# Kernel tuning notes

Measured on AMD Instinct MI355X. Metric: run time of the kernel, lower is better.

## Reference

```python
import jax, jax.numpy as jnp
import numpy as np

D_H, HEAD, LAYER_IDX = 1024, 16, 11
D_ATTN = D_H // HEAD
BZ, LEN = 2, 2048


def setup_inputs() -> dict:
    key = jax.random.key(0)
    ks = jax.random.split(key, 8)
    s = 1.0 / np.sqrt(D_H)
    v = jax.random.normal(ks[0], (BZ, LEN, D_H), jnp.float32)
    k = jax.random.normal(ks[1], (BZ, LEN, D_H), jnp.float32)
    q = jax.random.normal(ks[2], (BZ, LEN, D_H), jnp.float32)
    # causal mask: 1.0 where attention is blocked (j > i)
    causal = jnp.triu(jnp.ones((LEN, LEN), jnp.float32), k=1)
    mask = jnp.broadcast_to(causal[None, None], (BZ, 1, LEN, LEN))
    Wv = jax.random.normal(ks[3], (D_H, D_H), jnp.float32) * s
    Wk = jax.random.normal(ks[4], (D_H, D_H), jnp.float32) * s
    Wq = jax.random.normal(ks[5], (D_H, D_H), jnp.float32) * s
    Wo = jax.random.normal(ks[6], (D_H, D_H), jnp.float32) * s
    bo = jnp.zeros((D_H,), jnp.float32)
    return {"v": v, "k": k, "q": q, "mask": mask,
            "Wv": Wv, "Wk": Wk, "Wq": Wq, "Wo": Wo, "bo": bo}


def _split_head(x):
    # (bz, len, d_h) -> (bz, head, len, d_attn)
    bz, L, _ = x.shape
    return x.reshape(bz, L, HEAD, D_ATTN).transpose(0, 2, 1, 3)


def reference(v, k, q, mask, Wv, Wk, Wq, Wo, bo):
    bz, len_q, _ = q.shape
    vh = _split_head(v @ Wv)  # (bz, head, len_k, d_attn)
    kh = _split_head(k @ Wk)
    qh = _split_head(q @ Wq)
    scale = 1.0 / jnp.sqrt(jnp.asarray(D_ATTN, jnp.float32))
    weight = jnp.einsum("bhqd,bhkd->bhqk", qh, kh) * scale
    weight = weight + mask * (-1e9)
    weight = weight / jnp.asarray(LAYER_IDX + 1, jnp.float32)
    attn = jax.nn.softmax(weight, axis=-1)  # dropout omitted (inference)
    out = jnp.einsum("bhqk,bhkd->bhqd", attn, vh)
    out = out.transpose(0, 2, 1, 3).reshape(bz, len_q, D_H)
    return out @ Wo + bo
```

## Files before the change

### kernel.cpp

```cpp
#include <hip/hip_runtime.h>
#include <hip/hip_fp16.h>

typedef _Float16 f16;
typedef _Float16 f16x4 __attribute__((ext_vector_type(4)));
typedef _Float16 f16x8 __attribute__((ext_vector_type(8)));
typedef float f32x4 __attribute__((ext_vector_type(4)));

#define D_H   1024
#define LEN   2048
#define BZ    2
#define NHEAD 16
#define DA    64
#define MTOK  (BZ * LEN)
#define KDIM  1024
#define ATT_SCALE (0.125f / 12.0f)

__device__ __forceinline__ void load_lds16(const f16* g, f16* l) {
  __builtin_amdgcn_global_load_lds((const __attribute__((address_space(1))) void*)g,
                                   (__attribute__((address_space(3))) void*)l,
                                   16, 0, 0);
}

#define FENCE() __asm__ volatile("" ::: "memory")

__global__ __launch_bounds__(256)
void k_prep(const float* __restrict__ W0, const float* __restrict__ W1,
            const float* __restrict__ W2, const float* __restrict__ W3,
            const float* __restrict__ xq, const float* __restrict__ xk,
            const float* __restrict__ xv,
            f16* __restrict__ T0, f16* __restrict__ T1,
            f16* __restrict__ T2, f16* __restrict__ T3,
            f16* __restrict__ q16, f16* __restrict__ k16,
            f16* __restrict__ v16) {
  const int z = blockIdx.z;
  const int tx = threadIdx.x, ty = threadIdx.y;
  if (z < 4) {
    const float* W = (z == 0) ? W0 : (z == 1) ? W1 : (z == 2) ? W2 : W3;
    f16* Wt = (z == 0) ? T0 : (z == 1) ? T1 : (z == 2) ? T2 : T3;
    __shared__ float tile[32][33];
    int bx = blockIdx.x, by = blockIdx.y;
#pragma unroll
    for (int s = 0; s < 4; ++s)
      tile[ty + 8 * s][tx] = W[(size_t)(by * 32 + ty + 8 * s) * D_H + bx * 32 + tx];
    __syncthreads();
#pragma unroll
    for (int s = 0; s < 4; ++s)
      Wt[(size_t)(bx * 32 + ty + 8 * s) * D_H + by * 32 + tx] =
          (f16)tile[tx][ty + 8 * s];
  } else {
    const float* in = (z == 4) ? xq : (z == 5) ? xk : xv;
    f16* out = (z == 4) ? q16 : (z == 5) ? k16 : v16;
    int tid = ty * 32 + tx;
    size_t base = ((size_t)(blockIdx.y * 32 + blockIdx.x)) * 4096 + tid * 16;
#pragma unroll
    for (int s = 0; s < 4; ++s) {
      float4 x = *(const float4*)(in + base + s * 4);
      f16x4 o; o[0] = (f16)x.x; o[1] = (f16)x.y; o[2] = (f16)x.z; o[3] = (f16)x.w;
      *(f16x4*)(out + base + s * 4) = o;
    }
  }
}

#define BM2 256
#define BN2 256
#define BKT 64
#define NKT (KDIM / BKT)

__global__ __launch_bounds__(512, 2)
void k_gemm3(const f16* __restrict__ A0, const f16* __restrict__ A1,
             const f16* __restrict__ A2, const f16* __restrict__ W0,
             const f16* __restrict__ W1, const f16* __restrict__ W2,
             f16* __restrict__ O0, f16* __restrict__ O1, f16* __restrict__ O2) {
  __shared__ __align__(16) f16 smem3[65536];
  f16* As = smem3;
  f16* Bs = smem3 + 32768;
  const int z = blockIdx.z;
  const f16* A = (z == 0) ? A0 : (z == 1) ? A1 : A2;
  const f16* Bt = (z == 0) ? W0 : (z == 1) ? W1 : W2;
  f16* Out = (z == 0) ? O0 : (z == 1) ? O1 : O2;
  const int m0 = blockIdx.x * BM2, n0 = blockIdx.y * BN2;
  const int tid = threadIdx.x;
  const int wave = tid >> 6, lane = tid & 63;
  const int lc = lane & 15, quad = lane >> 4;
  const int wr = wave >> 2, wc = wave & 3;
  const f16* Ab = A + (size_t)m0 * KDIM;
  const f16* Bb = Bt + (size_t)n0 * KDIM;

  f32x4 acc[8][4] = {};

#define STAGE_HALF(g, ldsbase, kt, h)                                         \
  {                                                                           \
    _Pragma("unroll")                                                         \
    for (int r = 0; r < 2; ++r) {                                             \
      int idx = tid + r * 512;                                                \
      int row = (h) * 128 + (idx >> 3);                                       \
      int gch = (idx & 7) ^ (row & 7);                                        \
      load_lds16((g) + (size_t)row * KDIM + (kt) * BKT + gch * 8,             \
                 (ldsbase) + (h) * 8192 + idx * 8);                           \
    }                                                                         \
  }

#define READ_A(mh, kc)                                                        \
  _Pragma("unroll")                                                           \
  for (int i = 0; i < 4; ++i) {                                               \
    int row = wr * 128 + ((mh) * 4 + i) * 16 + lc;                            \
    int pc = ((kc) * 4 + quad) ^ (row & 7);                                   \
    af[i] = *(const f16x8*)&Ad[row * 64 + pc * 8];                            \
  }
#define READ_B(kc)                                                            \
  _Pragma("unroll")                                                           \
  for (int n = 0; n < 4; ++n) {                                               \
    int row = wc * 64 + n * 16 + lc;                                          \
    int pc = ((kc) * 4 + quad) ^ (row & 7);                                   \
    bf[n] = *(const f16x8*)&Bd[row * 64 + pc * 8];                            \
  }
#define MFMA_Q(mh)                                                            \
  FENCE(); __builtin_amdgcn_s_barrier();                                      \
  __asm__ volatile("s_waitcnt lgkmcnt(0)" ::: "memory");                      \
  __builtin_amdgcn_sched_barrier(0);                                          \
  __builtin_amdgcn_s_setprio(1);                                              \
  _Pragma("unroll")                                                           \
  for (int i = 0; i < 4; ++i)                                                 \
    _Pragma("unroll")                                                         \
    for (int n = 0; n < 4; ++n)                                               \
      acc[(mh) * 4 + i][n] = __builtin_amdgcn_mfma_f32_16x16x32_f16(          \
          af[i], bf[n], acc[(mh) * 4 + i][n], 0, 0, 0);                       \
  __builtin_amdgcn_s_setprio(0);                                              \
  FENCE(); __builtin_amdgcn_s_barrier(); FENCE();

  STAGE_HALF(Ab, As, 0, 0);
  STAGE_HALF(Ab, As, 0, 1);
  STAGE_HALF(Bb, Bs, 0, 0);
  STAGE_HALF(Bb, Bs, 0, 1);
  STAGE_HALF(Ab, As + 16384, 1, 0);
  __asm__ volatile("s_waitcnt vmcnt(2)" ::: "memory");
  __builtin_amdgcn_s_barrier();
  FENCE();

  for (int t = 0; t < NKT; ++t) {
    const f16* Ad = As + (t & 1) * 16384;
    const f16* Bd = Bs + (t & 1) * 16384;
    f16* AdW = As + (t & 1) * 16384;
    f16* Adn = As + ((t + 1) & 1) * 16384;
    f16* Bdn = Bs + ((t + 1) & 1) * 16384;
    const bool pf = (t + 1 < NKT);
    f16x8 af[4], bf[4];

    READ_A(0, 0); READ_B(0);
    if (pf) STAGE_HALF(Ab, Adn, t + 1, 1);
    MFMA_Q(0);

    READ_A(1, 0);
    if (pf) STAGE_HALF(Bb, Bdn, t + 1, 0);
    MFMA_Q(1);

    READ_A(0, 1); READ_B(1);
    if (pf) STAGE_HALF(Bb, Bdn, t + 1, 1);
    MFMA_Q(0);

    READ_A(1, 1);
    FENCE(); __builtin_amdgcn_s_barrier();
    __asm__ volatile("s_waitcnt lgkmcnt(0)" ::: "memory");
    __builtin_amdgcn_sched_barrier(0);
    __builtin_amdgcn_s_setprio(1);
#pragma unroll
    for (int i = 0; i < 4; ++i)
#pragma unroll
      for (int n = 0; n < 4; ++n)
        acc[4 + i][n] = __builtin_amdgcn_mfma_f32_16x16x32_f16(
            af[i], bf[n], acc[4 + i][n], 0, 0, 0);
    __builtin_amdgcn_s_setprio(0);
    if (t + 2 < NKT) {
      STAGE_HALF(Ab, AdW, t + 2, 0);
      __asm__ volatile("s_waitcnt vmcnt(2)" ::: "memory");
    } else if (pf) {
      __asm__ volatile("s_waitcnt vmcnt(0)" ::: "memory");
    }
    FENCE(); __builtin_amdgcn_s_barrier(); FENCE();
  }

  if (z <= 1) {
    f16* slice = smem3 + wave * 8192;
#pragma unroll
    for (int mi = 0; mi < 8; ++mi)
#pragma unroll
      for (int ni = 0; ni < 4; ++ni)
#pragma unroll
        for (int rr = 0; rr < 4; ++rr) {
          int tl = mi * 16 + quad * 4 + rr;
          int d = ni * 16 + lc;
          slice[tl * 64 + (((d >> 3) ^ (tl & 7)) << 3) + (d & 7)] =
              (f16)acc[mi][ni][rr];
        }
    __asm__ volatile("s_waitcnt lgkmcnt(0)" ::: "memory");
    const int h = (n0 >> 6) + wc;
    const int tokbase = m0 + wr * 128;
    const int b = tokbase >> 11, ib = tokbase & 2047;
#pragma unroll
    for (int s = 0; s < 16; ++s) {
      int u = lane + s * 64;
      int tl = u >> 3, ch = u & 7;
      f16x8 vv = *(const f16x8*)&slice[tl * 64 + ((ch ^ (tl & 7)) << 3)];
      *(f16x8*)(Out + ((size_t)((b << 4) + h) * LEN + ib + tl) * DA + ch * 8) = vv;
    }
  } else {
    f16* Ct = smem3;
#pragma unroll
    for (int e = 0; e < 2; ++e) {
      __syncthreads();
      if (wr == e) {
#pragma unroll
        for (int mi = 0; mi < 8; ++mi)
#pragma unroll
          for (int ni = 0; ni < 4; ++ni)
#pragma unroll
            for (int rr = 0; rr < 4; ++rr) {
              int tl = mi * 16 + quad * 4 + rr;
              int dl = wc * 64 + ni * 16 + lc;
              Ct[dl * 136 + tl] = (f16)acc[mi][ni][rr];
            }
      }
      __syncthreads();
      const int tokbase = m0 + e * 128;
      const int b = tokbase >> 11, j0 = tokbase & 2047;
#pragma unroll
      for (int s = 0; s < 8; ++s) {
        int u = tid + s * 512;
        int dl = u >> 4, ch = u & 15;
        f16x8 vv = *(const f16x8*)&Ct[dl * 136 + ch * 8];
        *(f16x8*)(Out + ((size_t)(b * 1024 + n0 + dl)) * LEN + j0 + ch * 8) = vv;
      }
    }
  }
}

#define OM 64
#define ON 128
#define BK 64
#define ONIT (KDIM / BK)
__global__ __launch_bounds__(256)
void k_gemm_out(const f16* __restrict__ A, const f16* __restrict__ Bt,
                float* __restrict__ Out, const float* __restrict__ bias) {
  __shared__ __align__(16) char smem[2 * (OM + ON) * BK * 2];
  f16* As = (f16*)smem;
  f16* Bs = As + 2 * OM * BK;
  const int m0 = blockIdx.x * OM, n0 = blockIdx.y * ON;
  const int tid = threadIdx.x;
  const int wave = tid >> 6, lane = tid & 63;
  const int lc = lane & 15, quad = lane >> 4;
  const int wm = (wave >> 1) * 32, wn = (wave & 1) * 64;
  const int swz = lc & 7;
  const f16* Abase = A + (size_t)m0 * KDIM;
  const f16* Bbase = Bt + (size_t)n0 * KDIM;

  f32x4 acc[2][4] = {};

#define STAGE_OUT(t)                                                          \
  {                                                                           \
    int k0s = (t) * BK;                                                       \
    f16* Ad = As + ((t) & 1) * (OM * BK);                                     \
    f16* Bd = Bs + ((t) & 1) * (ON * BK);                                     \
    _Pragma("unroll")                                                         \
    for (int r = 0; r < 2; ++r) {                                             \
      int idx = tid + r * 256;                                                \
      int row = idx >> 3, ch = idx & 7;                                       \
      int gch = ch ^ (row & 7);                                               \
      load_lds16(Abase + (size_t)row * KDIM + k0s + gch * 8, &Ad[idx * 8]);   \
    }                                                                         \
    _Pragma("unroll")                                                         \
    for (int r = 0; r < 4; ++r) {                                             \
      int idx = tid + r * 256;                                                \
      int row = idx >> 3, ch = idx & 7;                                       \
      int gch = ch ^ (row & 7);                                               \
      load_lds16(Bbase + (size_t)row * KDIM + k0s + gch * 8, &Bd[idx * 8]);   \
    }                                                                         \
  }

  STAGE_OUT(0);
  for (int t = 0; t < ONIT; ++t) {
    __syncthreads();
    if (t + 1 < ONIT) STAGE_OUT(t + 1);
    const f16* Ad = As + (t & 1) * (OM * BK);
    const f16* Bd = Bs + (t & 1) * (ON * BK);
#pragma unroll
    for (int kc = 0; kc < 2; ++kc) {
      f16x8 af[2], bf[4];
#pragma unroll
      for (int mi = 0; mi < 2; ++mi)
        af[mi] = *(const f16x8*)&Ad[(wm + mi * 16 + lc) * 64 +
                                    (((kc * 4 + quad) ^ swz) * 8)];
#pragma unroll
      for (int ni = 0; ni < 4; ++ni)
        bf[ni] = *(const f16x8*)&Bd[(wn + ni * 16 + lc) * 64 +
                                    (((kc * 4 + quad) ^ swz) * 8)];
#pragma unroll
      for (int mi = 0; mi < 2; ++mi)
#pragma unroll
        for (int ni = 0; ni < 4; ++ni)
          acc[mi][ni] = __builtin_amdgcn_mfma_f32_16x16x32_f16(
              af[mi], bf[ni], acc[mi][ni], 0, 0, 0);
    }
  }

  float* Ct = (float*)smem;
#pragma unroll
  for (int hf = 0; hf < 2; ++hf) {
    __syncthreads();
    if ((wave & 1) == hf) {
#pragma unroll
      for (int mi = 0; mi < 2; ++mi)
#pragma unroll
        for (int ni = 0; ni < 4; ++ni)
#pragma unroll
          for (int r = 0; r < 4; ++r) {
            int tok = wm + mi * 16 + quad * 4 + r;
            int d = ni * 16 + lc;
            Ct[tok * 68 + d] = acc[mi][ni][r];
          }
    }
    __syncthreads();
#pragma unroll
    for (int it = 0; it < 4; ++it) {
      int u = tid + it * 256;
      int tok = u >> 4, ch = u & 15;
      int gm = m0 + tok;
      int gc = n0 + hf * 64 + ch * 4;
      float4 bv = *(const float4*)(bias + gc);
      float4 cv = *(const float4*)&Ct[tok * 68 + ch * 4];
      float4 ov;
      ov.x = cv.x + bv.x; ov.y = cv.y + bv.y;
      ov.z = cv.z + bv.z; ov.w = cv.w + bv.w;
      *(float4*)(Out + (size_t)gm * D_H + gc) = ov;
    }
  }
}

__global__ __launch_bounds__(256, 4)
void k_attn(const f16* __restrict__ Qh, const f16* __restrict__ Kh,
            const f16* __restrict__ Vt, f16* __restrict__ O16) {
  __shared__ f16 Ks[2][64 * 64];
  __shared__ f16 Vs[2][64 * 64];
  __shared__ f16 Pw[4][16 * 64];
  const int tid = threadIdx.x;
  const int wave = tid >> 6, lane = tid & 63;
  const int lc = lane & 15, quad = lane >> 4;
  const int swz = lc & 7;
  const int bh = blockIdx.x & 31;
  const int qb = 31 - (blockIdx.x >> 5);
  const int i0 = qb * 64 + wave * 16;
  const int b = bh >> 4, h = bh & 15;
  const f16* Qb = Qh + (size_t)bh * LEN * DA;
  const f16* Kb = Kh + (size_t)bh * LEN * DA;
  const f16* Vb = Vt + (size_t)bh * DA * LEN;

  f16x8 aQ[2];
  const f16 qs = (f16)ATT_SCALE;
#pragma unroll
  for (int c = 0; c < 2; ++c) {
    aQ[c] = *(const f16x8*)(Qb + (size_t)(i0 + lc) * DA + c * 32 + quad * 8);
#pragma unroll
    for (int j = 0; j < 8; ++j) aQ[c][j] = aQ[c][j] * qs;
  }

  float lsum = 0.f;
  f32x4 accO[4] = {};
  f16* P = &Pw[wave][0];

  const int niter = qb + 1;

#pragma unroll
  for (int r = 0; r < 2; ++r) {
    int idx = tid + r * 256;
    int row = idx >> 3, ch = idx & 7;
    int gch = ch ^ (row & 7);
    load_lds16(Kb + (size_t)row * DA + gch * 8, &Ks[0][idx * 8]);
  }
#pragma unroll
  for (int r = 0; r < 2; ++r) {
    int idx = tid + r * 256;
    int row = idx >> 3, ch = idx & 7;
    int gch = ch ^ (row & 7);
    load_lds16(Vb + (size_t)row * LEN + gch * 8, &Vs[0][idx * 8]);
  }

  for (int t = 0; t < niter; ++t) {
    __syncthreads();
    if (t + 1 < niter) {
      int j0n = (t + 1) * 64, nb = (t + 1) & 1;
#pragma unroll
      for (int r = 0; r < 2; ++r) {
        int idx = tid + r * 256;
        int row = idx >> 3, ch = idx & 7;
        int gch = ch ^ (row & 7);
        load_lds16(Kb + (size_t)(j0n + row) * DA + gch * 8, &Ks[nb][idx * 8]);
      }
#pragma unroll
      for (int r = 0; r < 2; ++r) {
        int idx = tid + r * 256;
        int row = idx >> 3, ch = idx & 7;
        int gch = ch ^ (row & 7);
        load_lds16(Vb + (size_t)row * LEN + j0n + gch * 8, &Vs[nb][idx * 8]);
      }
    }
    const f16* ks = Ks[t & 1];
    const f16* vs = Vs[t & 1];

    f32x4 st[4] = {};
#pragma unroll
    for (int g = 0; g < 4; ++g)
#pragma unroll
      for (int c = 0; c < 2; ++c) {
        f16x8 aK = *(const f16x8*)&ks[(g * 16 + lc) * 64 +
                                      (((c * 4 + quad) ^ swz) * 8)];
        st[g] = __builtin_amdgcn_mfma_f32_16x16x32_f16(aK, aQ[c], st[g], 0, 0, 0);
      }
    float ev[4][4];
    if (t == niter - 1) {
      const int j0 = t * 64, q = i0 + lc;
#pragma unroll
      for (int g = 0; g < 4; ++g)
#pragma unroll
        for (int r = 0; r < 4; ++r) {
          int key = j0 + g * 16 + quad * 4 + r;
          float e = __expf(st[g][r]);
          e = (key > q) ? 0.f : e;
          lsum += e;
          ev[g][r] = e;
        }
    } else {
#pragma unroll
      for (int g = 0; g < 4; ++g)
#pragma unroll
        for (int r = 0; r < 4; ++r) {
          float e = __expf(st[g][r]);
          lsum += e;
          ev[g][r] = e;
        }
    }
#pragma unroll
    for (int g = 0; g < 4; ++g) {
      int c8 = ((g << 1) + (quad >> 1)) ^ swz;
      f16x4 pk;
      pk[0] = (f16)ev[g][0]; pk[1] = (f16)ev[g][1];
      pk[2] = (f16)ev[g][2]; pk[3] = (f16)ev[g][3];
      *(f16x4*)&P[lc * 64 + c8 * 8 + (quad & 1) * 4] = pk;
    }
    __asm__ volatile("s_waitcnt lgkmcnt(0)" ::: "memory");
    f16x8 aP[2];
#pragma unroll
    for (int c = 0; c < 2; ++c) {
      int c8 = (quad + 4 * c) ^ swz;
      aP[c] = *(const f16x8*)&P[lc * 64 + c8 * 8];
    }
#pragma unroll
    for (int dc = 0; dc < 4; ++dc) {
      f16x8 bV0 = *(const f16x8*)&vs[(dc * 16 + lc) * 64 + ((quad ^ swz) * 8)];
      f16x8 bV1 = *(const f16x8*)&vs[(dc * 16 + lc) * 64 + (((4 + quad) ^ swz) * 8)];
      accO[dc] = __builtin_amdgcn_mfma_f32_16x16x32_f16(aP[0], bV0, accO[dc], 0, 0, 0);
      accO[dc] = __builtin_amdgcn_mfma_f32_16x16x32_f16(aP[1], bV1, accO[dc], 0, 0, 0);
    }
  }

  lsum += __shfl_xor(lsum, 16, 64);
  lsum += __shfl_xor(lsum, 32, 64);
  float ls[4];
#pragma unroll
  for (int r = 0; r < 4; ++r) ls[r] = __shfl(lsum, quad * 4 + r, 64);

#pragma unroll
  for (int dc = 0; dc < 4; ++dc)
#pragma unroll
    for (int r = 0; r < 4; ++r) {
      int i = i0 + quad * 4 + r;
      int d = dc * 16 + lc;
      float v = accO[dc][r] / ls[r];
      O16[((size_t)(b * LEN + i)) * D_H + h * DA + d] = (f16)v;
    }
}

extern "C" void kernel_launch(void* const* d_in, const int* in_sizes, int n_in,
                              void* d_out, int out_size, void* d_ws, size_t ws_size,
                              hipStream_t stream) {
  const float* v_f = (const float*)d_in[0];
  const float* k_f = (const float*)d_in[1];
  const float* q_f = (const float*)d_in[2];
  const float* Wv = (const float*)d_in[4];
  const float* Wk = (const float*)d_in[5];
  const float* Wq = (const float*)d_in[6];
  const float* Wo = (const float*)d_in[7];
  const float* bo = (const float*)d_in[8];
  float* out = (float*)d_out;

  const size_t SZ_X = (size_t)MTOK * D_H;
  const size_t SZ_W = (size_t)D_H * D_H;
  f16* ws = (f16*)d_ws;
  f16* q16 = ws;
  f16* k16 = ws + SZ_X;
  f16* v16 = ws + 2 * SZ_X;
  f16* Qh  = ws + 3 * SZ_X;
  f16* Kh  = ws + 4 * SZ_X;
  f16* Vt  = ws + 5 * SZ_X;
  f16* Wqt = ws + 6 * SZ_X;
  f16* Wkt = Wqt + SZ_W;
  f16* Wvt = Wqt + 2 * SZ_W;
  f16* Wot = Wqt + 3 * SZ_W;
  f16* O16 = q16;

  k_prep<<<dim3(32, 32, 7), dim3(32, 8), 0, stream>>>(
      Wq, Wk, Wv, Wo, q_f, k_f, v_f, Wqt, Wkt, Wvt, Wot, q16, k16, v16);

  k_gemm3<<<dim3(MTOK / BM2, D_H / BN2, 3), 512, 0, stream>>>(
      q16, k16, v16, Wqt, Wkt, Wvt, Qh, Kh, Vt);

  k_attn<<<dim3(32 * 32), 256, 0, stream>>>(Qh, Kh, Vt, O16);

  k_gemm_out<<<dim3(MTOK / OM, D_H / ON), 256, 0, stream>>>(O16, Wot, out, bo);
}
```

Measured before the change: 214.3 us.

## Use 128-query attention blocks with 8 waves sharing K/V tiles

Doubles the query tile per attention block from 64 to 128 rows by launching 512 threads (8 waves), so each K/V tile loaded into LDS is reused by twice as many waves. Each thread now issues one K and one V async load per tile instead of two each. Causal masking now covers the last two key tiles. Block scheduling interleaves long and short query blocks. This halves the grid to 512 blocks and may reduce occupancy or load balance, and waves in the lower half of the block do masked work on a fully masked final tile.

```diff
diff --git a/kernel.cpp b/kernel.cpp
--- a/kernel.cpp
+++ b/kernel.cpp
@@ -335,19 +335,20 @@
   }
 }
 
-__global__ __launch_bounds__(256, 4)
+__global__ __launch_bounds__(512, 4)
 void k_attn(const f16* __restrict__ Qh, const f16* __restrict__ Kh,
             const f16* __restrict__ Vt, f16* __restrict__ O16) {
   __shared__ f16 Ks[2][64 * 64];
   __shared__ f16 Vs[2][64 * 64];
-  __shared__ f16 Pw[4][16 * 64];
+  __shared__ f16 Pw[8][16 * 64];
   const int tid = threadIdx.x;
   const int wave = tid >> 6, lane = tid & 63;
   const int lc = lane & 15, quad = lane >> 4;
   const int swz = lc & 7;
   const int bh = blockIdx.x & 31;
-  const int qb = 31 - (blockIdx.x >> 5);
-  const int i0 = qb * 64 + wave * 16;
+  const int idx16 = blockIdx.x >> 5;
+  const int qb = (idx16 < 8) ? (15 - idx16) : (idx16 - 8);
+  const int i0 = qb * 128 + wave * 16;
   const int b = bh >> 4, h = bh & 15;
   const f16* Qb = Qh + (size_t)bh * LEN * DA;
   const f16* Kb = Kh + (size_t)bh * LEN * DA;
@@ -366,41 +367,23 @@
   f32x4 accO[4] = {};
   f16* P = &Pw[wave][0];
 
-  const int niter = qb + 1;
-
-#pragma unroll
-  for (int r = 0; r < 2; ++r) {
-    int idx = tid + r * 256;
-    int row = idx >> 3, ch = idx & 7;
+  const int niter = 2 * qb + 2;
+
+  {
+    int row = tid >> 3, ch = tid & 7;
     int gch = ch ^ (row & 7);
-    load_lds16(Kb + (size_t)row * DA + gch * 8, &Ks[0][idx * 8]);
-  }
-#pragma unroll
-  for (int r = 0; r < 2; ++r) {
-    int idx = tid + r * 256;
-    int row = idx >> 3, ch = idx & 7;
-    int gch = ch ^ (row & 7);
-    load_lds16(Vb + (size_t)row * LEN + gch * 8, &Vs[0][idx * 8]);
+    load_lds16(Kb + (size_t)row * DA + gch * 8, &Ks[0][tid * 8]);
+    load_lds16(Vb + (size_t)row * LEN + gch * 8, &Vs[0][tid * 8]);
   }
 
   for (int t = 0; t < niter; ++t) {
     __syncthreads();
     if (t + 1 < niter) {
       int j0n = (t + 1) * 64, nb = (t + 1) & 1;
-#pragma unroll
-      for (int r = 0; r < 2; ++r) {
-        int idx = tid + r * 256;
-        int row = idx >> 3, ch = idx & 7;
-        int gch = ch ^ (row & 7);
-        load_lds16(Kb + (size_t)(j0n + row) * DA + gch * 8, &Ks[nb][idx * 8]);
-      }
-#pragma unroll
-      for (int r = 0; r < 2; ++r) {
-        int idx = tid + r * 256;
-        int row = idx >> 3, ch = idx & 7;
-        int gch = ch ^ (row & 7);
-        load_lds16(Vb + (size_t)row * LEN + j0n + gch * 8, &Vs[nb][idx * 8]);
-      }
+      int row = tid >> 3, ch = tid & 7;
+      int gch = ch ^ (row & 7);
+      load_lds16(Kb + (size_t)(j0n + row) * DA + gch * 8, &Ks[nb][tid * 8]);
+      load_lds16(Vb + (size_t)row * LEN + j0n + gch * 8, &Vs[nb][tid * 8]);
     }
     const f16* ks = Ks[t & 1];
     const f16* vs = Vs[t & 1];
@@ -415,7 +398,7 @@
         st[g] = __builtin_amdgcn_mfma_f32_16x16x32_f16(aK, aQ[c], st[g], 0, 0, 0);
       }
     float ev[4][4];
-    if (t == niter - 1) {
+    if (t >= niter - 2) {
       const int j0 = t * 64, q = i0 + lc;
 #pragma unroll
       for (int g = 0; g < 4; ++g)
@@ -512,7 +495,7 @@
   k_gemm3<<<dim3(MTOK / BM2, D_H / BN2, 3), 512, 0, stream>>>(
       q16, k16, v16, Wqt, Wkt, Wvt, Qh, Kh, Vt);
 
-  k_attn<<<dim3(32 * 32), 256, 0, stream>>>(Qh, Kh, Vt, O16);
+  k_attn<<<dim3(32 * 16), 512, 0, stream>>>(Qh, Kh, Vt, O16);
 
   k_gemm_out<<<dim3(MTOK / OM, D_H / ON), 256, 0, stream>>>(O16, Wot, out, bo);
 }
```

Result: slower. 222.1 us (+3.6%).
